# Performance work log

Hardware: AMD Instinct MI355X
Metric: run time of the kernel (lower is better)

## Reference

```python
import jax, jax.numpy as jnp
import numpy as np

N_STATE = 64   # S4 state size N
L_MAX = 4096   # sequence length
H = 256        # number of SSM channels (d_model)
BATCH = 16


def _green_roots(Lambda, P, B, C, step, L):
    """Frequency-domain S4 kernel at the L roots of unity (Q = P, DPLR).
    Lambda,P,B,C: complex[N]; step: scalar. Returns complex[L]."""
    Omega = jnp.exp(-2j * jnp.pi * (jnp.arange(L) / L))          # (L,)
    g = (2.0 / step) * ((1.0 - Omega) / (1.0 + Omega))           # (L,)
    c = 2.0 / (1.0 + Omega)                                      # (L,)
    # four Cauchy numerators stacked: k00,k01,k10,k11
    vs = jnp.stack([C.conj() * B, C.conj() * P,
                    P.conj() * B, P.conj() * P])                 # (4,N)
    denom = g[:, None] - Lambda[None, :]                         # (L,N)
    k = jnp.einsum('kn,ln->kl', vs, 1.0 / denom)                 # (4,L)
    k00, k01, k10, k11 = k
    return c * (k00 - k01 * (1.0 / (1.0 + k11)) * k10)           # (L,)


def _kernel_freq(Lambda_re, Lambda_im, P_re, P_im, B_re, B_im,
                 C_re, C_im, log_step, L):
    Lambda = (Lambda_re + 1j * Lambda_im).astype(jnp.complex64)  # (H,N)
    P = (P_re + 1j * P_im).astype(jnp.complex64)
    Bm = (B_re + 1j * B_im).astype(jnp.complex64)
    Cm = (C_re + 1j * C_im).astype(jnp.complex64)
    step = jnp.exp(log_step)                                     # (H,)
    f = lambda lam, p, b, c, s: _green_roots(lam, p, b, c, s, L)
    return jax.vmap(f)(Lambda, P, Bm, Cm, step)                  # (H,L)


def setup_inputs() -> dict:
    key = jax.random.key(0)
    ks = jax.random.split(key, 10)
    u = jax.random.normal(ks[0], (BATCH, H, L_MAX), dtype=jnp.float32)
    # stable continuous-time poles: negative real part, spread imag parts
    Lambda_re = -0.5 * jnp.ones((H, N_STATE), jnp.float32) \
        - jax.random.uniform(ks[1], (H, N_STATE), dtype=jnp.float32)
    Lambda_im = jnp.pi * jax.random.normal(ks[2], (H, N_STATE), dtype=jnp.float32) * N_STATE / 8
    scale = 1.0 / np.sqrt(N_STATE)
    P_re = scale * jax.random.normal(ks[3], (H, N_STATE), dtype=jnp.float32)
    P_im = scale * jax.random.normal(ks[4], (H, N_STATE), dtype=jnp.float32)
    B_re = scale * jax.random.normal(ks[5], (H, N_STATE), dtype=jnp.float32)
    B_im = scale * jax.random.normal(ks[6], (H, N_STATE), dtype=jnp.float32)
    C_re = scale * jax.random.normal(ks[7], (H, N_STATE), dtype=jnp.float32)
    C_im = scale * jax.random.normal(ks[8], (H, N_STATE), dtype=jnp.float32)
    # log-uniform step in [1e-3, 1e-1] (log_step_initializer)
    log_step = (jax.random.uniform(ks[9], (H,), dtype=jnp.float32)
                * (np.log(0.1) - np.log(0.001)) + np.log(0.001)).astype(jnp.float32)
    return {"u": u, "Lambda_re": Lambda_re, "Lambda_im": Lambda_im,
            "P_re": P_re, "P_im": P_im, "B_re": B_re, "B_im": B_im,
            "C_re": C_re, "C_im": C_im, "log_step": log_step}


def reference(u, Lambda_re, Lambda_im, P_re, P_im, B_re, B_im,
              C_re, C_im, log_step):
    L = u.shape[-1]
    Kf = _kernel_freq(Lambda_re, Lambda_im, P_re, P_im, B_re, B_im,
                      C_re, C_im, log_step, L)                   # (H,L) complex
    # circular_convolution_complex, batched over (BATCH,H)
    ud = jnp.fft.fft(u, axis=-1)                                  # (B,H,L)
    y = jnp.fft.ifft(ud * Kf[None, :, :], n=L, axis=-1)
    return y.real.astype(jnp.float32)                             # (B,H,L)
```

## Files before the change

kernel.cpp:

```cpp
#include <hip/hip_runtime.h>
#include <math.h>

#define NSTATE 64
#define LEN    4096
#define NH     256
#define NB     16

typedef float f2 __attribute__((ext_vector_type(2)));

__device__ f2 g_ksym[NH * LEN];

__device__ __forceinline__ int rev8_12(int p) {
  return ((p & 7) << 9) | (((p >> 3) & 7) << 6) | (((p >> 6) & 7) << 3) | (p >> 9);
}

__device__ __forceinline__ f2 mkf2(float a, float b){ f2 r; r.x = a; r.y = b; return r; }

__device__ __forceinline__ f2 cmul_pk(f2 a, f2 b) {
  f2 t, r;
  asm("v_pk_mul_f32 %0, %1, %2 op_sel:[0,0] op_sel_hi:[0,1]"
      : "=v"(t) : "v"(a), "v"(b));
  asm("v_pk_fma_f32 %0, %1, %2, %3 op_sel:[1,1,0] op_sel_hi:[1,0,1] neg_lo:[0,1,0]"
      : "=v"(r) : "v"(a), "v"(b), "v"(t));
  return r;
}
__device__ __forceinline__ f2 cmulc_pk(f2 a, f2 b) {
  f2 t, r;
  asm("v_pk_mul_f32 %0, %1, %2 op_sel:[0,0] op_sel_hi:[0,1] neg_hi:[0,1]"
      : "=v"(t) : "v"(a), "v"(b));
  asm("v_pk_fma_f32 %0, %1, %2, %3 op_sel:[1,1,0] op_sel_hi:[1,0,1]"
      : "=v"(r) : "v"(a), "v"(b), "v"(t));
  return r;
}
__device__ __forceinline__ void cmac_pk(f2& acc, f2 v, f2 e) {
  asm("v_pk_fma_f32 %0, %1, %2, %0 op_sel:[0,0,0] op_sel_hi:[0,1,1]"
      : "+v"(acc) : "v"(v), "v"(e));
  asm("v_pk_fma_f32 %0, %1, %2, %0 op_sel:[1,1,0] op_sel_hi:[1,0,1] neg_lo:[0,1,0]"
      : "+v"(acc) : "v"(v), "v"(e));
}
__device__ __forceinline__ void pk_fma(f2& acc, f2 a, f2 b) {
  asm("v_pk_fma_f32 %0, %1, %2, %0" : "+v"(acc) : "v"(a), "v"(b));
}

#define RSQ2 0.70710678118654752f

__device__ __forceinline__ void bfly8_fwd(f2 v[8]) {
  f2 a0 = v[0] + v[4], b0 = v[0] - v[4];
  f2 a1 = v[1] + v[5], d1 = v[1] - v[5];
  f2 a2 = v[2] + v[6], d2 = v[2] - v[6];
  f2 a3 = v[3] + v[7], d3 = v[3] - v[7];
  f2 b1 = mkf2(RSQ2 * (d1.x + d1.y), RSQ2 * (d1.y - d1.x));
  f2 b3 = mkf2(RSQ2 * (d3.y - d3.x), -RSQ2 * (d3.x + d3.y));
  f2 u0 = a0 + a2, u1 = a0 - a2, u2 = a1 + a3, u3 = a1 - a3;
  v[0] = u0 + u2;
  v[2] = mkf2(u1.x + u3.y, u1.y - u3.x);
  v[4] = u0 - u2;
  v[6] = mkf2(u1.x - u3.y, u1.y + u3.x);
  f2 w0 = mkf2(b0.x + d2.y, b0.y - d2.x);
  f2 w1 = mkf2(b0.x - d2.y, b0.y + d2.x);
  f2 w2 = b1 + b3, w3 = b1 - b3;
  v[1] = w0 + w2;
  v[3] = mkf2(w1.x + w3.y, w1.y - w3.x);
  v[5] = w0 - w2;
  v[7] = mkf2(w1.x - w3.y, w1.y + w3.x);
}

__device__ __forceinline__ void bfly8_inv(f2 v[8]) {
  f2 a0 = v[0] + v[4], b0 = v[0] - v[4];
  f2 a1 = v[1] + v[5], d1 = v[1] - v[5];
  f2 a2 = v[2] + v[6], d2 = v[2] - v[6];
  f2 a3 = v[3] + v[7], d3 = v[3] - v[7];
  f2 b1 = mkf2(RSQ2 * (d1.x - d1.y), RSQ2 * (d1.x + d1.y));
  f2 b3 = mkf2(-RSQ2 * (d3.x + d3.y), RSQ2 * (d3.x - d3.y));
  f2 u0 = a0 + a2, u1 = a0 - a2, u2 = a1 + a3, u3 = a1 - a3;
  v[0] = u0 + u2;
  v[2] = mkf2(u1.x - u3.y, u1.y + u3.x);
  v[4] = u0 - u2;
  v[6] = mkf2(u1.x + u3.y, u1.y - u3.x);
  f2 w0 = mkf2(b0.x - d2.y, b0.y + d2.x);
  f2 w1 = mkf2(b0.x + d2.y, b0.y - d2.x);
  f2 w2 = b1 + b3, w3 = b1 - b3;
  v[1] = w0 + w2;
  v[3] = mkf2(w1.x - w3.y, w1.y + w3.x);
  v[5] = w0 - w2;
  v[7] = mkf2(w1.x + w3.y, w1.y - w3.x);
}

__device__ __forceinline__ void twiddle7(f2 v[8], f2 w1) {
  f2 w2 = cmul_pk(w1, w1);
  f2 w3 = cmul_pk(w2, w1);
  f2 w4 = cmul_pk(w2, w2);
  f2 w5 = cmul_pk(w3, w2);
  f2 w6 = cmul_pk(w3, w3);
  f2 w7 = cmul_pk(w4, w3);
  v[1] = cmul_pk(v[1], w1); v[2] = cmul_pk(v[2], w2); v[3] = cmul_pk(v[3], w3);
  v[4] = cmul_pk(v[4], w4); v[5] = cmul_pk(v[5], w5); v[6] = cmul_pk(v[6], w6);
  v[7] = cmul_pk(v[7], w7);
}
__device__ __forceinline__ void twiddle7c(f2 v[8], f2 w1) {
  f2 w2 = cmul_pk(w1, w1);
  f2 w3 = cmul_pk(w2, w1);
  f2 w4 = cmul_pk(w2, w2);
  f2 w5 = cmul_pk(w3, w2);
  f2 w6 = cmul_pk(w3, w3);
  f2 w7 = cmul_pk(w4, w3);
  v[1] = cmulc_pk(v[1], w1); v[2] = cmulc_pk(v[2], w2); v[3] = cmulc_pk(v[3], w3);
  v[4] = cmulc_pk(v[4], w4); v[5] = cmulc_pk(v[5], w5); v[6] = cmulc_pk(v[6], w6);
  v[7] = cmulc_pk(v[7], w7);
}

#define WAVE_SYNC() asm volatile("s_waitcnt lgkmcnt(0)" ::: "memory")

__global__ __launch_bounds__(256) void s4_kernel_freq(
    const float* __restrict__ Lre, const float* __restrict__ Lim,
    const float* __restrict__ Pre, const float* __restrict__ Pim,
    const float* __restrict__ Bre, const float* __restrict__ Bim,
    const float* __restrict__ Cre, const float* __restrict__ Cim,
    const float* __restrict__ log_step)
{
  __shared__ float4 sLam[NSTATE];
  __shared__ float4 sV01[NSTATE];
  __shared__ f2     sV2[NSTATE];

  const int blk = blockIdx.x;
  const int h = blk >> 3;
  const int j = ((blk & 7) << 8) | threadIdx.x;

  if (threadIdx.x < NSTATE) {
    int idx = h * NSTATE + threadIdx.x;
    float lr = Lre[idx], li = Lim[idx];
    float pr = Pre[idx], pi = Pim[idx];
    float br = Bre[idx], bi = Bim[idx];
    float cr = Cre[idx], ci = Cim[idx];
    float pp = pr * pr + pi * pi;
    sLam[threadIdx.x] = make_float4(lr, li, pp, pp);
    sV01[threadIdx.x] = make_float4(cr * br + ci * bi, cr * bi - ci * br,
                                    cr * pr + ci * pi, cr * pi - ci * pr);
    sV2[threadIdx.x] = mkf2(pr * br + pi * bi, pr * bi - pi * br);
  }

  const float step = expf(log_step[h]);
  const float ts = 2.0f / step;
  const float NEG2PI = -6.2831853071795864769f;

  float gar, gai, car, cai, gbr, gbi, cbr, cbi;
  {
    float so, co;
    sincosf(NEG2PI * ((float)j * (1.0f / (float)LEN)), &so, &co);
    float dr = 1.0f + co, di = so;
    float inv = 1.0f / fmaf(dr, dr, di * di);
    car = 2.0f * dr * inv; cai = -2.0f * di * inv;
    float nr = 1.0f - co, ni = -so;
    gar = ts * (fmaf(nr, dr, ni * di) * inv);
    gai = ts * (fmaf(ni, dr, -nr * di) * inv);
  }
  if (j == 0) {
    float so, co;
    sincosf(NEG2PI * 0.5f, &so, &co);
    float dr = 1.0f + co, di = so;
    float inv = 1.0f / fmaf(dr, dr, di * di);
    cbr = 2.0f * dr * inv; cbi = -2.0f * di * inv;
    float nr = 1.0f - co, ni = -so;
    gbr = ts * (fmaf(nr, dr, ni * di) * inv);
    gbi = ts * (fmaf(ni, dr, -nr * di) * inv);
  } else {
    gbr = gar; gbi = -gai; cbr = car; cbi = -cai;
  }
  const f2 gA = mkf2(gar, gai);
  const f2 gB = mkf2(gbr, gbi);

  f2 A00 = {0,0}, A01 = {0,0}, A10 = {0,0}, A11 = {0,0};
  f2 B00 = {0,0}, B01 = {0,0}, B10 = {0,0}, B11 = {0,0};

  __syncthreads();

#pragma unroll 8
  for (int n = 0; n < NSTATE; ++n) {
    float4 L4 = sLam[n];
    float4 V4 = sV01[n];
    f2 v2 = sV2[n];
    f2 lam = mkf2(L4.x, L4.y);
    f2 pp  = mkf2(L4.z, L4.w);
    f2 v0  = mkf2(V4.x, V4.y);
    f2 v1  = mkf2(V4.z, V4.w);
    {
      f2 d = gA - lam;
      float idn = __builtin_amdgcn_rcpf(fmaf(d.x, d.x, d.y * d.y));
      f2 e = mkf2(d.x * idn, -(d.y * idn));
      cmac_pk(A00, v0, e); cmac_pk(A01, v1, e);
      cmac_pk(A10, v2, e); pk_fma(A11, pp, e);
    }
    {
      f2 d = gB - lam;
      float idn = __builtin_amdgcn_rcpf(fmaf(d.x, d.x, d.y * d.y));
      f2 e = mkf2(d.x * idn, -(d.y * idn));
      cmac_pk(B00, v0, e); cmac_pk(B01, v1, e);
      cmac_pk(B10, v2, e); pk_fma(B11, pp, e);
    }
  }

#define FINISH(cr_, ci_, k00,k01,k10,k11, Kr, Ki)                            \
  {                                                                          \
    float rr = 1.0f + k11.x, ri = k11.y;                                     \
    float rinv = 1.0f / fmaf(rr, rr, ri * ri);                               \
    float pr_ = k01.x * k10.x - k01.y * k10.y;                               \
    float pi_ = k01.x * k10.y + k01.y * k10.x;                               \
    float wr = (pr_ * rr + pi_ * ri) * rinv;                                 \
    float wi = (pi_ * rr - pr_ * ri) * rinv;                                 \
    float sr = k00.x - wr, si = k00.y - wi;                                  \
    Kr = cr_ * sr - ci_ * si; Ki = cr_ * si + ci_ * sr;                      \
  }

  float Kar, Kai, Kbr, Kbi;
  FINISH(car, cai, A00, A01, A10, A11, Kar, Kai)
  FINISH(cbr, cbi, B00, B01, B10, B11, Kbr, Kbi)
#undef FINISH

  f2* out = g_ksym + (size_t)h * LEN;
  if (j == 0) {
    out[rev8_12(0)]    = mkf2(Kar, 0.0f);
    out[rev8_12(2048)] = mkf2(Kbr, 0.0f);
  } else {
    float fr = 0.5f * (Kar + Kbr), fi = 0.5f * (Kai - Kbi);
    out[rev8_12(j)]       = mkf2(fr, fi);
    out[rev8_12(LEN - j)] = mkf2(fr, -fi);
  }
}

__global__ __launch_bounds__(512) void s4_fftconv(const float* __restrict__ u,
                                                 float* __restrict__ y)
{
  __shared__ f2 X[4608];

  const int t = threadIdx.x;
  const int bid = blockIdx.x;
  const int h  = bid & (NH - 1);
  const int bp = bid >> 8;

  const int w  = t >> 6;
  const int i  = t & 63;
  const int i3 = i >> 3;
  const int i7 = i & 7;
  const int R  = 576 * w;

  float c1, s1, c2, s2, c3, s3;
  sincosf((float)t  * (-6.2831853071795864769f / 4096.0f), &s1, &c1);
  sincosf((float)i  * (-6.2831853071795864769f /  512.0f), &s2, &c2);
  sincosf((float)i7 * (-6.2831853071795864769f /   64.0f), &s3, &c3);
  const f2 W1 = mkf2(c1, s1), W2 = mkf2(c2, s2), W3 = mkf2(c3, s3);

  const float* u1 = u + ((size_t)bp * NH + h) * LEN;
  const float* u2 = u + ((size_t)(bp + 8) * NH + h) * LEN;

  f2 v[8];
#pragma unroll
  for (int m = 0; m < 8; ++m)
    v[m] = mkf2(u1[t + 512 * m], u2[t + 512 * m]);
  bfly8_fwd(v);
  twiddle7(v, W1);
#pragma unroll
  for (int m = 0; m < 8; ++m) X[576 * m + t] = v[m];
  __syncthreads();

#pragma unroll
  for (int m = 0; m < 8; ++m) v[m] = X[R + i + 64 * m];
  bfly8_fwd(v);
  twiddle7(v, W2);
#pragma unroll
  for (int m = 0; m < 8; ++m) X[R + 68 * m + i] = v[m];
  WAVE_SYNC();

#pragma unroll
  for (int m = 0; m < 8; ++m) v[m] = X[R + 68 * i3 + i7 + 8 * m];
  bfly8_fwd(v);
  twiddle7(v, W3);
#pragma unroll
  for (int m = 0; m < 8; ++m) X[R + 9 * (8 * i3 + m) + i7] = v[m];
  WAVE_SYNC();

  {
    const float4* kp = (const float4*)(g_ksym + (size_t)h * LEN + 8 * t);
    float4 k0 = kp[0], k1 = kp[1], k2 = kp[2], k3 = kp[3];
#pragma unroll
    for (int m = 0; m < 8; ++m) v[m] = X[R + 9 * i + m];
    bfly8_fwd(v);
    v[0] = cmul_pk(v[0], mkf2(k0.x, k0.y));
    v[1] = cmul_pk(v[1], mkf2(k0.z, k0.w));
    v[2] = cmul_pk(v[2], mkf2(k1.x, k1.y));
    v[3] = cmul_pk(v[3], mkf2(k1.z, k1.w));
    v[4] = cmul_pk(v[4], mkf2(k2.x, k2.y));
    v[5] = cmul_pk(v[5], mkf2(k2.z, k2.w));
    v[6] = cmul_pk(v[6], mkf2(k3.x, k3.y));
    v[7] = cmul_pk(v[7], mkf2(k3.z, k3.w));
    bfly8_inv(v);
#pragma unroll
    for (int p = 0; p < 8; ++p) X[R + 9 * i + p] = v[p];
  }
  WAVE_SYNC();

#pragma unroll
  for (int m = 0; m < 8; ++m) v[m] = X[R + 9 * (8 * i3 + m) + i7];
  twiddle7c(v, W3);
  bfly8_inv(v);
#pragma unroll
  for (int p = 0; p < 8; ++p) X[R + 68 * i3 + i7 + 8 * p] = v[p];
  WAVE_SYNC();

#pragma unroll
  for (int m = 0; m < 8; ++m) v[m] = X[R + 68 * m + i];
  twiddle7c(v, W2);
  bfly8_inv(v);
#pragma unroll
  for (int p = 0; p < 8; ++p) X[R + i + 64 * p] = v[p];
  __syncthreads();

#pragma unroll
  for (int m = 0; m < 8; ++m) v[m] = X[576 * m + t];
  twiddle7c(v, W1);
  bfly8_inv(v);

  float* y1 = y + ((size_t)bp * NH + h) * LEN;
  float* y2 = y + ((size_t)(bp + 8) * NH + h) * LEN;
  const float sc = 1.0f / (float)LEN;
#pragma unroll
  for (int p = 0; p < 8; ++p) {
    y1[t + 512 * p] = v[p].x * sc;
    y2[t + 512 * p] = v[p].y * sc;
  }
}

extern "C" void kernel_launch(void* const* d_in, const int* in_sizes, int n_in,
                              void* d_out, int out_size, void* d_ws, size_t ws_size,
                              hipStream_t stream) {
  const float* u    = (const float*)d_in[0];
  const float* Lre  = (const float*)d_in[1];
  const float* Lim  = (const float*)d_in[2];
  const float* Pre  = (const float*)d_in[3];
  const float* Pim  = (const float*)d_in[4];
  const float* Bre  = (const float*)d_in[5];
  const float* Bim  = (const float*)d_in[6];
  const float* Cre  = (const float*)d_in[7];
  const float* Cim  = (const float*)d_in[8];
  const float* lstep = (const float*)d_in[9];
  float* y = (float*)d_out;

  s4_kernel_freq<<<NH * 8, 256, 0, stream>>>(Lre, Lim, Pre, Pim, Bre, Bim, Cre, Cim, lstep);
  s4_fftconv<<<NH * (NB / 2), 512, 0, stream>>>(u, y);
}
```

Measured before the change: 175.4 us.

## Process four batch rows per FFT block with swizzled float4 LDS layout

The FFT convolution block now packs two complex pairs (four real sequences) per thread into float4 shared memory, so each block handles four batches per channel and reuses one load of the kernel spectrum across them. Padded strides are replaced with XOR swizzles. The per-state precomputation moves into a separate prep kernel writing global buffers that the kernel-frequency stage reads directly, instead of staging through shared memory. This doubles register use and LDS per block and halves the grid size, and it adds an extra kernel launch.

```diff
diff --git a/kernel.cpp b/kernel.cpp
--- a/kernel.cpp
+++ b/kernel.cpp
@@ -9,6 +9,9 @@
 typedef float f2 __attribute__((ext_vector_type(2)));
 
 __device__ f2 g_ksym[NH * LEN];
+__device__ float4 g_pA[NH * NSTATE];
+__device__ float4 g_pB[NH * NSTATE];
+__device__ float2 g_pC[NH * NSTATE];
 
 __device__ __forceinline__ int rev8_12(int p) {
   return ((p & 7) << 9) | (((p >> 3) & 7) << 6) | (((p >> 6) & 7) << 3) | (p >> 9);
@@ -86,58 +89,52 @@
   v[7] = mkf2(w1.x + w3.y, w1.y - w3.x);
 }
 
-__device__ __forceinline__ void twiddle7(f2 v[8], f2 w1) {
-  f2 w2 = cmul_pk(w1, w1);
-  f2 w3 = cmul_pk(w2, w1);
-  f2 w4 = cmul_pk(w2, w2);
-  f2 w5 = cmul_pk(w3, w2);
-  f2 w6 = cmul_pk(w3, w3);
-  f2 w7 = cmul_pk(w4, w3);
-  v[1] = cmul_pk(v[1], w1); v[2] = cmul_pk(v[2], w2); v[3] = cmul_pk(v[3], w3);
-  v[4] = cmul_pk(v[4], w4); v[5] = cmul_pk(v[5], w5); v[6] = cmul_pk(v[6], w6);
-  v[7] = cmul_pk(v[7], w7);
-}
-__device__ __forceinline__ void twiddle7c(f2 v[8], f2 w1) {
-  f2 w2 = cmul_pk(w1, w1);
-  f2 w3 = cmul_pk(w2, w1);
-  f2 w4 = cmul_pk(w2, w2);
-  f2 w5 = cmul_pk(w3, w2);
-  f2 w6 = cmul_pk(w3, w3);
-  f2 w7 = cmul_pk(w4, w3);
-  v[1] = cmulc_pk(v[1], w1); v[2] = cmulc_pk(v[2], w2); v[3] = cmulc_pk(v[3], w3);
-  v[4] = cmulc_pk(v[4], w4); v[5] = cmulc_pk(v[5], w5); v[6] = cmulc_pk(v[6], w6);
-  v[7] = cmulc_pk(v[7], w7);
+__device__ __forceinline__ void twiddle7x2(f2 va[8], f2 vb[8], f2 w1) {
+  f2 w2 = cmul_pk(w1, w1), w3 = cmul_pk(w2, w1), w4 = cmul_pk(w2, w2),
+     w5 = cmul_pk(w3, w2), w6 = cmul_pk(w3, w3), w7 = cmul_pk(w4, w3);
+  va[1] = cmul_pk(va[1], w1); va[2] = cmul_pk(va[2], w2); va[3] = cmul_pk(va[3], w3);
+  va[4] = cmul_pk(va[4], w4); va[5] = cmul_pk(va[5], w5); va[6] = cmul_pk(va[6], w6);
+  va[7] = cmul_pk(va[7], w7);
+  vb[1] = cmul_pk(vb[1], w1); vb[2] = cmul_pk(vb[2], w2); vb[3] = cmul_pk(vb[3], w3);
+  vb[4] = cmul_pk(vb[4], w4); vb[5] = cmul_pk(vb[5], w5); vb[6] = cmul_pk(vb[6], w6);
+  vb[7] = cmul_pk(vb[7], w7);
+}
+__device__ __forceinline__ void twiddle7x2c(f2 va[8], f2 vb[8], f2 w1) {
+  f2 w2 = cmul_pk(w1, w1), w3 = cmul_pk(w2, w1), w4 = cmul_pk(w2, w2),
+     w5 = cmul_pk(w3, w2), w6 = cmul_pk(w3, w3), w7 = cmul_pk(w4, w3);
+  va[1] = cmulc_pk(va[1], w1); va[2] = cmulc_pk(va[2], w2); va[3] = cmulc_pk(va[3], w3);
+  va[4] = cmulc_pk(va[4], w4); va[5] = cmulc_pk(va[5], w5); va[6] = cmulc_pk(va[6], w6);
+  va[7] = cmulc_pk(va[7], w7);
+  vb[1] = cmulc_pk(vb[1], w1); vb[2] = cmulc_pk(vb[2], w2); vb[3] = cmulc_pk(vb[3], w3);
+  vb[4] = cmulc_pk(vb[4], w4); vb[5] = cmulc_pk(vb[5], w5); vb[6] = cmulc_pk(vb[6], w6);
+  vb[7] = cmulc_pk(vb[7], w7);
 }
 
 #define WAVE_SYNC() asm volatile("s_waitcnt lgkmcnt(0)" ::: "memory")
 
-__global__ __launch_bounds__(256) void s4_kernel_freq(
+__global__ __launch_bounds__(256) void s4_prep(
     const float* __restrict__ Lre, const float* __restrict__ Lim,
     const float* __restrict__ Pre, const float* __restrict__ Pim,
     const float* __restrict__ Bre, const float* __restrict__ Bim,
-    const float* __restrict__ Cre, const float* __restrict__ Cim,
-    const float* __restrict__ log_step)
+    const float* __restrict__ Cre, const float* __restrict__ Cim)
 {
-  __shared__ float4 sLam[NSTATE];
-  __shared__ float4 sV01[NSTATE];
-  __shared__ f2     sV2[NSTATE];
-
+  int idx = blockIdx.x * 256 + threadIdx.x;
+  if (idx >= NH * NSTATE) return;
+  float lr = Lre[idx], li = Lim[idx];
+  float pr = Pre[idx], pi = Pim[idx];
+  float br = Bre[idx], bi = Bim[idx];
+  float cr = Cre[idx], ci = Cim[idx];
+  g_pA[idx] = make_float4(lr, li, pr * pr + pi * pi, 0.0f);
+  g_pB[idx] = make_float4(cr * br + ci * bi, cr * bi - ci * br,
+                          cr * pr + ci * pi, cr * pi - ci * pr);
+  g_pC[idx] = make_float2(pr * br + pi * bi, pr * bi - pi * br);
+}
+
+__global__ __launch_bounds__(256) void s4_kernel_freq(const float* __restrict__ log_step)
+{
   const int blk = blockIdx.x;
   const int h = blk >> 3;
   const int j = ((blk & 7) << 8) | threadIdx.x;
-
-  if (threadIdx.x < NSTATE) {
-    int idx = h * NSTATE + threadIdx.x;
-    float lr = Lre[idx], li = Lim[idx];
-    float pr = Pre[idx], pi = Pim[idx];
-    float br = Bre[idx], bi = Bim[idx];
-    float cr = Cre[idx], ci = Cim[idx];
-    float pp = pr * pr + pi * pi;
-    sLam[threadIdx.x] = make_float4(lr, li, pp, pp);
-    sV01[threadIdx.x] = make_float4(cr * br + ci * bi, cr * bi - ci * br,
-                                    cr * pr + ci * pi, cr * pi - ci * pr);
-    sV2[threadIdx.x] = mkf2(pr * br + pi * bi, pr * bi - pi * br);
-  }
 
   const float step = expf(log_step[h]);
   const float ts = 2.0f / step;
@@ -172,17 +169,20 @@
   f2 A00 = {0,0}, A01 = {0,0}, A10 = {0,0}, A11 = {0,0};
   f2 B00 = {0,0}, B01 = {0,0}, B10 = {0,0}, B11 = {0,0};
 
-  __syncthreads();
+  const float4* __restrict__ pa = g_pA + h * NSTATE;
+  const float4* __restrict__ pb = g_pB + h * NSTATE;
+  const float2* __restrict__ pc = g_pC + h * NSTATE;
 
 #pragma unroll 8
   for (int n = 0; n < NSTATE; ++n) {
-    float4 L4 = sLam[n];
-    float4 V4 = sV01[n];
-    f2 v2 = sV2[n];
+    float4 L4 = pa[n];
+    float4 V4 = pb[n];
+    float2 C2 = pc[n];
     f2 lam = mkf2(L4.x, L4.y);
-    f2 pp  = mkf2(L4.z, L4.w);
+    f2 pp  = mkf2(L4.z, L4.z);
     f2 v0  = mkf2(V4.x, V4.y);
     f2 v1  = mkf2(V4.z, V4.w);
+    f2 v2  = mkf2(C2.x, C2.y);
     {
       f2 d = gA - lam;
       float idn = __builtin_amdgcn_rcpf(fmaf(d.x, d.x, d.y * d.y));
@@ -227,21 +227,20 @@
   }
 }
 
-__global__ __launch_bounds__(512) void s4_fftconv(const float* __restrict__ u,
-                                                 float* __restrict__ y)
+__global__ __launch_bounds__(512, 4) void s4_fftconv(const float* __restrict__ u,
+                                                    float* __restrict__ y)
 {
-  __shared__ f2 X[4608];
+  __shared__ float4 X[4096];
 
   const int t = threadIdx.x;
   const int bid = blockIdx.x;
   const int h  = bid & (NH - 1);
-  const int bp = bid >> 8;
+  const int q  = bid >> 8;
 
   const int w  = t >> 6;
   const int i  = t & 63;
   const int i3 = i >> 3;
   const int i7 = i & 7;
-  const int R  = 576 * w;
 
   float c1, s1, c2, s2, c3, s3;
   sincosf((float)t  * (-6.2831853071795864769f / 4096.0f), &s1, &c1);
@@ -249,83 +248,132 @@
   sincosf((float)i7 * (-6.2831853071795864769f /   64.0f), &s3, &c3);
   const f2 W1 = mkf2(c1, s1), W2 = mkf2(c2, s2), W3 = mkf2(c3, s3);
 
-  const float* u1 = u + ((size_t)bp * NH + h) * LEN;
-  const float* u2 = u + ((size_t)(bp + 8) * NH + h) * LEN;
-
-  f2 v[8];
-#pragma unroll
-  for (int m = 0; m < 8; ++m)
-    v[m] = mkf2(u1[t + 512 * m], u2[t + 512 * m]);
-  bfly8_fwd(v);
-  twiddle7(v, W1);
-#pragma unroll
-  for (int m = 0; m < 8; ++m) X[576 * m + t] = v[m];
+  const float* uA1 = u + ((size_t)q        * NH + h) * LEN;
+  const float* uA2 = u + ((size_t)(q + 8)  * NH + h) * LEN;
+  const float* uB1 = u + ((size_t)(q + 4)  * NH + h) * LEN;
+  const float* uB2 = u + ((size_t)(q + 12) * NH + h) * LEN;
+
+  f2 va[8], vb[8];
+#pragma unroll
+  for (int m = 0; m < 8; ++m) {
+    va[m] = mkf2(uA1[t + 512 * m], uA2[t + 512 * m]);
+    vb[m] = mkf2(uB1[t + 512 * m], uB2[t + 512 * m]);
+  }
+  bfly8_fwd(va); bfly8_fwd(vb);
+  twiddle7x2(va, vb, W1);
+  const int base1 = t ^ ((t >> 3) & 7);
+#pragma unroll
+  for (int m = 0; m < 8; ++m)
+    X[512 * m + base1] = make_float4(va[m].x, va[m].y, vb[m].x, vb[m].y);
+
+  const float4* kp = (const float4*)(g_ksym + (size_t)h * LEN + 8 * t);
+  float4 k0 = kp[0], k1 = kp[1], k2 = kp[2], k3 = kp[3];
   __syncthreads();
 
-#pragma unroll
-  for (int m = 0; m < 8; ++m) v[m] = X[R + i + 64 * m];
-  bfly8_fwd(v);
-  twiddle7(v, W2);
-#pragma unroll
-  for (int m = 0; m < 8; ++m) X[R + 68 * m + i] = v[m];
+  const int base2 = 512 * w + (i ^ i3);
+#pragma unroll
+  for (int m = 0; m < 8; ++m) {
+    float4 xv = X[base2 + 64 * m];
+    va[m] = mkf2(xv.x, xv.y); vb[m] = mkf2(xv.z, xv.w);
+  }
+  bfly8_fwd(va); bfly8_fwd(vb);
+  twiddle7x2(va, vb, W2);
+#pragma unroll
+  for (int m = 0; m < 8; ++m)
+    X[base2 + 64 * m] = make_float4(va[m].x, va[m].y, vb[m].x, vb[m].y);
   WAVE_SYNC();
 
-#pragma unroll
-  for (int m = 0; m < 8; ++m) v[m] = X[R + 68 * i3 + i7 + 8 * m];
-  bfly8_fwd(v);
-  twiddle7(v, W3);
-#pragma unroll
-  for (int m = 0; m < 8; ++m) X[R + 9 * (8 * i3 + m) + i7] = v[m];
+  int a3[8];
+  {
+    const int b3 = 512 * w + 64 * i3;
+#pragma unroll
+    for (int m = 0; m < 8; ++m) a3[m] = b3 + 8 * m + (i7 ^ m);
+  }
+#pragma unroll
+  for (int m = 0; m < 8; ++m) {
+    float4 xv = X[a3[m]];
+    va[m] = mkf2(xv.x, xv.y); vb[m] = mkf2(xv.z, xv.w);
+  }
+  bfly8_fwd(va); bfly8_fwd(vb);
+  twiddle7x2(va, vb, W3);
+#pragma unroll
+  for (int m = 0; m < 8; ++m)
+    X[a3[m]] = make_float4(va[m].x, va[m].y, vb[m].x, vb[m].y);
   WAVE_SYNC();
 
+  int a4[8];
   {
-    const float4* kp = (const float4*)(g_ksym + (size_t)h * LEN + 8 * t);
-    float4 k0 = kp[0], k1 = kp[1], k2 = kp[2], k3 = kp[3];
-#pragma unroll
-    for (int m = 0; m < 8; ++m) v[m] = X[R + 9 * i + m];
-    bfly8_fwd(v);
-    v[0] = cmul_pk(v[0], mkf2(k0.x, k0.y));
-    v[1] = cmul_pk(v[1], mkf2(k0.z, k0.w));
-    v[2] = cmul_pk(v[2], mkf2(k1.x, k1.y));
-    v[3] = cmul_pk(v[3], mkf2(k1.z, k1.w));
-    v[4] = cmul_pk(v[4], mkf2(k2.x, k2.y));
-    v[5] = cmul_pk(v[5], mkf2(k2.z, k2.w));
-    v[6] = cmul_pk(v[6], mkf2(k3.x, k3.y));
-    v[7] = cmul_pk(v[7], mkf2(k3.z, k3.w));
-    bfly8_inv(v);
-#pragma unroll
-    for (int p = 0; p < 8; ++p) X[R + 9 * i + p] = v[p];
-  }
+    const int b4 = 512 * w + 8 * i;
+#pragma unroll
+    for (int m = 0; m < 8; ++m) a4[m] = b4 + (m ^ i7);
+  }
+#pragma unroll
+  for (int m = 0; m < 8; ++m) {
+    float4 xv = X[a4[m]];
+    va[m] = mkf2(xv.x, xv.y); vb[m] = mkf2(xv.z, xv.w);
+  }
+  bfly8_fwd(va); bfly8_fwd(vb);
+  {
+    f2 kk0 = mkf2(k0.x,k0.y), kk1 = mkf2(k0.z,k0.w), kk2 = mkf2(k1.x,k1.y), kk3 = mkf2(k1.z,k1.w);
+    f2 kk4 = mkf2(k2.x,k2.y), kk5 = mkf2(k2.z,k2.w), kk6 = mkf2(k3.x,k3.y), kk7 = mkf2(k3.z,k3.w);
+    va[0] = cmul_pk(va[0], kk0); vb[0] = cmul_pk(vb[0], kk0);
+    va[1] = cmul_pk(va[1], kk1); vb[1] = cmul_pk(vb[1], kk1);
+    va[2] = cmul_pk(va[2], kk2); vb[2] = cmul_pk(vb[2], kk2);
+    va[3] = cmul_pk(va[3], kk3); vb[3] = cmul_pk(vb[3], kk3);
+    va[4] = cmul_pk(va[4], kk4); vb[4] = cmul_pk(vb[4], kk4);
+    va[5] = cmul_pk(va[5], kk5); vb[5] = cmul_pk(vb[5], kk5);
+    va[6] = cmul_pk(va[6], kk6); vb[6] = cmul_pk(vb[6], kk6);
+    va[7] = cmul_pk(va[7], kk7); vb[7] = cmul_pk(vb[7], kk7);
+  }
+  bfly8_inv(va); bfly8_inv(vb);
+#pragma unroll
+  for (int m = 0; m < 8; ++m)
+    X[a4[m]] = make_float4(va[m].x, va[m].y, vb[m].x, vb[m].y);
   WAVE_SYNC();
 
 #pragma unroll
-  for (int m = 0; m < 8; ++m) v[m] = X[R + 9 * (8 * i3 + m) + i7];
-  twiddle7c(v, W3);
-  bfly8_inv(v);
-#pragma unroll
-  for (int p = 0; p < 8; ++p) X[R + 68 * i3 + i7 + 8 * p] = v[p];
+  for (int m = 0; m < 8; ++m) {
+    float4 xv = X[a3[m]];
+    va[m] = mkf2(xv.x, xv.y); vb[m] = mkf2(xv.z, xv.w);
+  }
+  twiddle7x2c(va, vb, W3);
+  bfly8_inv(va); bfly8_inv(vb);
+#pragma unroll
+  for (int m = 0; m < 8; ++m)
+    X[a3[m]] = make_float4(va[m].x, va[m].y, vb[m].x, vb[m].y);
   WAVE_SYNC();
 
 #pragma unroll
-  for (int m = 0; m < 8; ++m) v[m] = X[R + 68 * m + i];
-  twiddle7c(v, W2);
-  bfly8_inv(v);
-#pragma unroll
-  for (int p = 0; p < 8; ++p) X[R + i + 64 * p] = v[p];
+  for (int m = 0; m < 8; ++m) {
+    float4 xv = X[base2 + 64 * m];
+    va[m] = mkf2(xv.x, xv.y); vb[m] = mkf2(xv.z, xv.w);
+  }
+  twiddle7x2c(va, vb, W2);
+  bfly8_inv(va); bfly8_inv(vb);
+#pragma unroll
+  for (int m = 0; m < 8; ++m)
+    X[base2 + 64 * m] = make_float4(va[m].x, va[m].y, vb[m].x, vb[m].y);
   __syncthreads();
 
 #pragma unroll
-  for (int m = 0; m < 8; ++m) v[m] = X[576 * m + t];
-  twiddle7c(v, W1);
-  bfly8_inv(v);
-
-  float* y1 = y + ((size_t)bp * NH + h) * LEN;
-  float* y2 = y + ((size_t)(bp + 8) * NH + h) * LEN;
+  for (int m = 0; m < 8; ++m) {
+    float4 xv = X[512 * m + base1];
+    va[m] = mkf2(xv.x, xv.y); vb[m] = mkf2(xv.z, xv.w);
+  }
+  twiddle7x2c(va, vb, W1);
+  bfly8_inv(va); bfly8_inv(vb);
+
+  float* yA1 = y + ((size_t)q        * NH + h) * LEN;
+  float* yA2 = y + ((size_t)(q + 8)  * NH + h) * LEN;
+  float* yB1 = y + ((size_t)(q + 4)  * NH + h) * LEN;
+  float* yB2 = y + ((size_t)(q + 12) * NH + h) * LEN;
   const float sc = 1.0f / (float)LEN;
 #pragma unroll
   for (int p = 0; p < 8; ++p) {
-    y1[t + 512 * p] = v[p].x * sc;
-    y2[t + 512 * p] = v[p].y * sc;
+    yA1[t + 512 * p] = va[p].x * sc;
+    yA2[t + 512 * p] = va[p].y * sc;
+    yB1[t + 512 * p] = vb[p].x * sc;
+    yB2[t + 512 * p] = vb[p].y * sc;
   }
 }
 
@@ -344,6 +392,7 @@
   const float* lstep = (const float*)d_in[9];
   float* y = (float*)d_out;
 
-  s4_kernel_freq<<<NH * 8, 256, 0, stream>>>(Lre, Lim, Pre, Pim, Bre, Bim, Cre, Cim, lstep);
-  s4_fftconv<<<NH * (NB / 2), 512, 0, stream>>>(u, y);
-}
+  s4_prep<<<(NH * NSTATE + 255) / 256, 256, 0, stream>>>(Lre, Lim, Pre, Pim, Bre, Bim, Cre, Cim);
+  s4_kernel_freq<<<NH * 8, 256, 0, stream>>>(lstep);
+  s4_fftconv<<<NH * 4, 512, 0, stream>>>(u, y);
+}
```

New measurement: 190.2 us. 1.08x slower.

## Compute four frequency points per thread in Cauchy kernel; prefetch K earlier

Applied to the files above, without the earlier changes.

Each thread of the Cauchy kernel now evaluates four frequency points (q, its conjugate, q+1024 and its conjugate) instead of two. This halves the number of blocks and amortizes the shared-memory loads of Lambda and the Cauchy numerators over more work. Separately, the FFT-conv kernel issues its global loads of the frequency-domain kernel before the first barrier so their latency overlaps the butterfly stages. The cost is higher register pressure from 16 complex accumulators and less parallelism in the kernel-generation launch.

```diff
diff --git a/kernel.cpp b/kernel.cpp
--- a/kernel.cpp
+++ b/kernel.cpp
@@ -123,8 +123,8 @@
   __shared__ f2     sV2[NSTATE];
 
   const int blk = blockIdx.x;
-  const int h = blk >> 3;
-  const int j = ((blk & 7) << 8) | threadIdx.x;
+  const int h = blk >> 2;
+  const int q = ((blk & 3) << 8) | threadIdx.x;
 
   if (threadIdx.x < NSTATE) {
     int idx = h * NSTATE + threadIdx.x;
@@ -144,9 +144,10 @@
   const float NEG2PI = -6.2831853071795864769f;
 
   float gar, gai, car, cai, gbr, gbi, cbr, cbi;
+  float gcr, gci, ccr, cci, gdr, gdi, cdr, cdi;
   {
     float so, co;
-    sincosf(NEG2PI * ((float)j * (1.0f / (float)LEN)), &so, &co);
+    sincosf(NEG2PI * ((float)q * (1.0f / (float)LEN)), &so, &co);
     float dr = 1.0f + co, di = so;
     float inv = 1.0f / fmaf(dr, dr, di * di);
     car = 2.0f * dr * inv; cai = -2.0f * di * inv;
@@ -154,7 +155,7 @@
     gar = ts * (fmaf(nr, dr, ni * di) * inv);
     gai = ts * (fmaf(ni, dr, -nr * di) * inv);
   }
-  if (j == 0) {
+  if (q == 0) {
     float so, co;
     sincosf(NEG2PI * 0.5f, &so, &co);
     float dr = 1.0f + co, di = so;
@@ -166,15 +167,38 @@
   } else {
     gbr = gar; gbi = -gai; cbr = car; cbi = -cai;
   }
-  const f2 gA = mkf2(gar, gai);
-  const f2 gB = mkf2(gbr, gbi);
+  {
+    float so, co;
+    sincosf(NEG2PI * ((float)(q + 1024) * (1.0f / (float)LEN)), &so, &co);
+    float dr = 1.0f + co, di = so;
+    float inv = 1.0f / fmaf(dr, dr, di * di);
+    ccr = 2.0f * dr * inv; cci = -2.0f * di * inv;
+    float nr = 1.0f - co, ni = -so;
+    gcr = ts * (fmaf(nr, dr, ni * di) * inv);
+    gci = ts * (fmaf(ni, dr, -nr * di) * inv);
+  }
+  gdr = gcr; gdi = -gci; cdr = ccr; cdi = -cci;
+
+  const f2 gA = mkf2(gar, gai), gB = mkf2(gbr, gbi);
+  const f2 gC = mkf2(gcr, gci), gD = mkf2(gdr, gdi);
 
   f2 A00 = {0,0}, A01 = {0,0}, A10 = {0,0}, A11 = {0,0};
   f2 B00 = {0,0}, B01 = {0,0}, B10 = {0,0}, B11 = {0,0};
+  f2 C00 = {0,0}, C01 = {0,0}, C10 = {0,0}, C11 = {0,0};
+  f2 D00 = {0,0}, D01 = {0,0}, D10 = {0,0}, D11 = {0,0};
 
   __syncthreads();
 
-#pragma unroll 8
+#define CAU(g_, k00,k01,k10,k11)                                             \
+  {                                                                          \
+    f2 d = g_ - lam;                                                         \
+    float idn = __builtin_amdgcn_rcpf(fmaf(d.x, d.x, d.y * d.y));            \
+    f2 e = mkf2(d.x * idn, -(d.y * idn));                                    \
+    cmac_pk(k00, v0, e); cmac_pk(k01, v1, e);                                \
+    cmac_pk(k10, v2, e); pk_fma(k11, pp, e);                                 \
+  }
+
+#pragma unroll 4
   for (int n = 0; n < NSTATE; ++n) {
     float4 L4 = sLam[n];
     float4 V4 = sV01[n];
@@ -183,21 +207,12 @@
     f2 pp  = mkf2(L4.z, L4.w);
     f2 v0  = mkf2(V4.x, V4.y);
     f2 v1  = mkf2(V4.z, V4.w);
-    {
-      f2 d = gA - lam;
-      float idn = __builtin_amdgcn_rcpf(fmaf(d.x, d.x, d.y * d.y));
-      f2 e = mkf2(d.x * idn, -(d.y * idn));
-      cmac_pk(A00, v0, e); cmac_pk(A01, v1, e);
-      cmac_pk(A10, v2, e); pk_fma(A11, pp, e);
-    }
-    {
-      f2 d = gB - lam;
-      float idn = __builtin_amdgcn_rcpf(fmaf(d.x, d.x, d.y * d.y));
-      f2 e = mkf2(d.x * idn, -(d.y * idn));
-      cmac_pk(B00, v0, e); cmac_pk(B01, v1, e);
-      cmac_pk(B10, v2, e); pk_fma(B11, pp, e);
-    }
-  }
+    CAU(gA, A00, A01, A10, A11)
+    CAU(gB, B00, B01, B10, B11)
+    CAU(gC, C00, C01, C10, C11)
+    CAU(gD, D00, D01, D10, D11)
+  }
+#undef CAU
 
 #define FINISH(cr_, ci_, k00,k01,k10,k11, Kr, Ki)                            \
   {                                                                          \
@@ -211,19 +226,26 @@
     Kr = cr_ * sr - ci_ * si; Ki = cr_ * si + ci_ * sr;                      \
   }
 
-  float Kar, Kai, Kbr, Kbi;
+  float Kar, Kai, Kbr, Kbi, Kcr, Kci, Kdr, Kdi;
   FINISH(car, cai, A00, A01, A10, A11, Kar, Kai)
   FINISH(cbr, cbi, B00, B01, B10, B11, Kbr, Kbi)
+  FINISH(ccr, cci, C00, C01, C10, C11, Kcr, Kci)
+  FINISH(cdr, cdi, D00, D01, D10, D11, Kdr, Kdi)
 #undef FINISH
 
   f2* out = g_ksym + (size_t)h * LEN;
-  if (j == 0) {
+  if (q == 0) {
     out[rev8_12(0)]    = mkf2(Kar, 0.0f);
     out[rev8_12(2048)] = mkf2(Kbr, 0.0f);
   } else {
     float fr = 0.5f * (Kar + Kbr), fi = 0.5f * (Kai - Kbi);
-    out[rev8_12(j)]       = mkf2(fr, fi);
-    out[rev8_12(LEN - j)] = mkf2(fr, -fi);
+    out[rev8_12(q)]        = mkf2(fr, fi);
+    out[rev8_12(LEN - q)]  = mkf2(fr, -fi);
+  }
+  {
+    float fr = 0.5f * (Kcr + Kdr), fi = 0.5f * (Kci - Kdi);
+    out[rev8_12(1024 + q)] = mkf2(fr, fi);
+    out[rev8_12(3072 - q)] = mkf2(fr, -fi);
   }
 }
 
@@ -260,6 +282,10 @@
   twiddle7(v, W1);
 #pragma unroll
   for (int m = 0; m < 8; ++m) X[576 * m + t] = v[m];
+
+  const float4* kp = (const float4*)(g_ksym + (size_t)h * LEN + 8 * t);
+  float4 k0 = kp[0], k1 = kp[1], k2 = kp[2], k3 = kp[3];
+
   __syncthreads();
 
 #pragma unroll
@@ -279,8 +305,6 @@
   WAVE_SYNC();
 
   {
-    const float4* kp = (const float4*)(g_ksym + (size_t)h * LEN + 8 * t);
-    float4 k0 = kp[0], k1 = kp[1], k2 = kp[2], k3 = kp[3];
 #pragma unroll
     for (int m = 0; m < 8; ++m) v[m] = X[R + 9 * i + m];
     bfly8_fwd(v);
@@ -344,6 +368,6 @@
   const float* lstep = (const float*)d_in[9];
   float* y = (float*)d_out;
 
-  s4_kernel_freq<<<NH * 8, 256, 0, stream>>>(Lre, Lim, Pre, Pim, Bre, Bim, Cre, Cim, lstep);
+  s4_kernel_freq<<<NH * 4, 256, 0, stream>>>(Lre, Lim, Pre, Pim, Bre, Bim, Cre, Cim, lstep);
   s4_fftconv<<<NH * (NB / 2), 512, 0, stream>>>(u, y);
 }
```

Result: faster. 171.9 us (-2.0%).
